# Kernel tuning notes

Measured on AMD Instinct MI355X. Metric: run time of the kernel, lower is better.

The kernel has to match this reference:

```python
import jax, jax.numpy as jnp
import numpy as np

B, S, D, F, E, K = 4, 2048, 512, 2048, 8, 2


def setup_inputs() -> dict:
    key = jax.random.key(0)
    kx, kg, kw, kv, k2 = jax.random.split(key, 5)
    scale = 0.02
    return {
        "x": jax.random.normal(kx, (B, S, D), dtype=jnp.float32),
        "Wg": jax.random.normal(kg, (D, E), dtype=jnp.float32) * scale,
        "W": jax.random.normal(kw, (E, D, F), dtype=jnp.float32) * scale,
        "V": jax.random.normal(kv, (E, D, F), dtype=jnp.float32) * scale,
        "W2": jax.random.normal(k2, (E, F, D), dtype=jnp.float32) * scale,
    }


def reference(x, Wg, W, V, W2):
    # Gating: top-k over expert logits, softmax over the selected k logits.
    gate_logits = jnp.einsum("bsd,de->bse", x, Wg)                 # [B,S,E]
    topv, topi = jax.lax.top_k(gate_logits, K)                      # [B,S,K]
    w = jax.nn.softmax(topv, axis=-1)                               # [B,S,K]
    # Dense per-token combine weights: gw[b,s,e] = sum_k w[b,s,k]*[topi[b,s,k]==e]
    gw = jnp.sum(w[..., None] * jax.nn.one_hot(topi, E, dtype=x.dtype), axis=-2)  # [B,S,E]

    y = jnp.zeros_like(x)
    n_experts = W.shape[0]
    for e in range(n_experts):  # fixed small loop over experts
        h = jax.nn.silu(jnp.einsum("bsd,df->bsf", x, W[e])) * jnp.einsum("bsd,df->bsf", x, V[e])
        y = y + gw[..., e:e + 1] * jnp.einsum("bsf,fd->bsd", h, W2[e])
    return y
```

## Files before the change

kernel.cpp:

```cpp
#include <hip/hip_runtime.h>
#include <hip/hip_bf16.h>
#include <stdint.h>

#define TT 8192
#define DD 512
#define FF 2048
#define EE 8
#define MAXT 136

typedef __attribute__((ext_vector_type(8))) short bf16x8;
typedef __attribute__((ext_vector_type(4))) float f32x4;

static __device__ __forceinline__ unsigned short f2b(float f) {
  union { __hip_bfloat16 b; unsigned short u; } cv;
  cv.b = __float2bfloat16(f);
  return cv.u;
}
static __device__ __forceinline__ float b2f(unsigned short u) {
  union { unsigned int i; float f; } cv;
  cv.i = ((unsigned int)u) << 16;
  return cv.f;
}

static __device__ __forceinline__ void gload16(const void* g, void* l) {
  __builtin_amdgcn_global_load_lds(
      (const __attribute__((address_space(1))) unsigned int*)g,
      (__attribute__((address_space(3))) unsigned int*)l, 16, 0, 0);
}

#define VMCNT12 asm volatile("s_waitcnt vmcnt(12)" ::: "memory")
#define VMCNT6  asm volatile("s_waitcnt vmcnt(6)" ::: "memory")
#define VMCNT0  asm volatile("s_waitcnt vmcnt(0)" ::: "memory")
#define BARX    asm volatile("s_barrier" ::: "memory")

__launch_bounds__(256)
__global__ void k_prep(const float* __restrict__ x, const float* __restrict__ Wg,
                       unsigned short* __restrict__ xb,
                       int* __restrict__ te, float* __restrict__ tw) {
  int wid = threadIdx.x >> 6, lane = threadIdx.x & 63;
  int t = blockIdx.x * 4 + wid;
  const float* xr = x + (size_t)t * DD;
  unsigned short* xbr = xb + (size_t)t * DD;
  int d0 = lane * 8;

  float4 v0 = *(const float4*)(xr + d0);
  float4 v1 = *(const float4*)(xr + d0 + 4);
  ushort4 o0, o1;
  o0.x = f2b(v0.x); o0.y = f2b(v0.y); o0.z = f2b(v0.z); o0.w = f2b(v0.w);
  o1.x = f2b(v1.x); o1.y = f2b(v1.y); o1.z = f2b(v1.z); o1.w = f2b(v1.w);
  *(ushort4*)(xbr + d0) = o0;
  *(ushort4*)(xbr + d0 + 4) = o1;

  float xv[8] = {v0.x, v0.y, v0.z, v0.w, v1.x, v1.y, v1.z, v1.w};
  float acc[EE];
#pragma unroll
  for (int e = 0; e < EE; e++) acc[e] = 0.f;
#pragma unroll
  for (int j = 0; j < 8; j++) {
    const float* wg = Wg + (size_t)(d0 + j) * EE;
    float4 a = *(const float4*)wg;
    float4 b = *(const float4*)(wg + 4);
    acc[0] += xv[j] * a.x; acc[1] += xv[j] * a.y; acc[2] += xv[j] * a.z; acc[3] += xv[j] * a.w;
    acc[4] += xv[j] * b.x; acc[5] += xv[j] * b.y; acc[6] += xv[j] * b.z; acc[7] += xv[j] * b.w;
  }
#pragma unroll
  for (int e = 0; e < EE; e++)
    for (int o = 32; o; o >>= 1) acc[e] += __shfl_xor(acc[e], o);
  if (lane == 0) {
    int e1 = 0; float v1m = acc[0];
#pragma unroll
    for (int e = 1; e < EE; e++) if (acc[e] > v1m) { v1m = acc[e]; e1 = e; }
    int e2 = -1; float v2m = -INFINITY;
#pragma unroll
    for (int e = 0; e < EE; e++) if (e != e1 && acc[e] > v2m) { v2m = acc[e]; e2 = e; }
    float ex = __expf(v2m - v1m);
    float w1 = 1.f / (1.f + ex);
    float w2 = ex / (1.f + ex);
    te[t * 2] = e1; te[t * 2 + 1] = e2;
    tw[t * 2] = w1; tw[t * 2 + 1] = w2;
  }
}

__global__ void k_tcvt_all(const float* __restrict__ W, const float* __restrict__ V,
                           const float* __restrict__ W2, unsigned short* __restrict__ Wt,
                           unsigned short* __restrict__ Vt, unsigned short* __restrict__ W2t) {
  __shared__ float tile[32][33];
  int z = blockIdx.y;
  const float* src; unsigned short* dst; int N, nbx;
  if (z < 16) {
    int e = z & 7;
    size_t base = (size_t)e * DD * FF;
    src = (z < 8 ? W : V) + base;
    dst = (z < 8 ? Wt : Vt) + base;
    N = FF; nbx = FF / 32;
  } else {
    int e = z - 16;
    size_t base = (size_t)e * DD * FF;
    src = W2 + base; dst = W2t + base;
    N = DD; nbx = DD / 32;
  }
  int M = (z < 16) ? DD : FF;
  int bx = blockIdx.x;
  int cb = (bx % nbx) * 32, rb = (bx / nbx) * 32;
  int tx = threadIdx.x, ty = threadIdx.y;
#pragma unroll
  for (int i = 0; i < 4; i++)
    tile[ty + i * 8][tx] = src[(size_t)(rb + ty + i * 8) * N + cb + tx];
  __syncthreads();
#pragma unroll
  for (int i = 0; i < 4; i++)
    dst[(size_t)(cb + ty + i * 8) * M + rb + tx] = f2b(tile[tx][ty + i * 8]);
}

__launch_bounds__(1024)
__global__ void k_route(const int* __restrict__ te, const float* __restrict__ tw,
                        int* __restrict__ ctrl, int* __restrict__ perm,
                        float* __restrict__ pw, int* __restrict__ tileE,
                        int* __restrict__ tileRow, int* __restrict__ inv) {
  __shared__ int wsum[17][EE];
  __shared__ int ebase[EE];
  int tid = threadIdx.x;
  int lane = tid & 63, wid = tid >> 6;
  int myte[16]; float mytw[16];
  int c[EE];
#pragma unroll
  for (int e = 0; e < EE; e++) c[e] = 0;
  int s0 = tid * 16;
#pragma unroll
  for (int j = 0; j < 16; j++) {
    myte[j] = te[s0 + j];
    mytw[j] = tw[s0 + j];
#pragma unroll
    for (int e = 0; e < EE; e++) if (myte[j] == e) c[e]++;
  }
  int incl[EE];
#pragma unroll
  for (int e = 0; e < EE; e++) incl[e] = c[e];
  for (int off = 1; off < 64; off <<= 1) {
#pragma unroll
    for (int e = 0; e < EE; e++) {
      int v = __shfl_up(incl[e], off);
      if (lane >= off) incl[e] += v;
    }
  }
  if (lane == 63)
#pragma unroll
    for (int e = 0; e < EE; e++) wsum[wid][e] = incl[e];
  __syncthreads();
  if (tid < EE) {
    int s = 0;
    for (int w = 0; w < 16; w++) { int v = wsum[w][tid]; wsum[w][tid] = s; s += v; }
    wsum[16][tid] = s;
  }
  __syncthreads();
  if (tid == 0) {
    int s = 0, nt = 0;
    for (int e = 0; e < EE; e++) {
      int cnt = wsum[16][e];
      ebase[e] = s; ctrl[8 + e] = s; ctrl[e] = cnt;
      for (int i = 0; i < cnt; i += 128) { tileE[nt] = e; tileRow[nt] = s + i; nt++; }
      s += cnt;
    }
    ctrl[16] = s; ctrl[17] = nt;
  }
  __syncthreads();
#pragma unroll
  for (int e = 0; e < EE; e++) {
    int p = ebase[e] + wsum[wid][e] + incl[e] - c[e];
#pragma unroll
    for (int j = 0; j < 16; j++) {
      if (myte[j] == e) {
        perm[p] = (s0 + j) >> 1;
        pw[p] = mytw[j];
        inv[s0 + j] = p;
        p++;
      }
    }
  }
}

__launch_bounds__(256, 2)
__global__ void k_ffn1(const unsigned short* __restrict__ xb,
                       const unsigned short* __restrict__ Wt,
                       const unsigned short* __restrict__ Vt,
                       const int* __restrict__ perm, const float* __restrict__ pw,
                       const int* __restrict__ ctrl, const int* __restrict__ tileE,
                       const int* __restrict__ tileRow,
                       unsigned short* __restrict__ h) {
  int ti = blockIdx.y;
  if (ti >= ctrl[17]) return;
  int e = tileE[ti];
  int row0 = tileRow[ti];
  int last = ctrl[8 + e] + ctrl[e] - 1;
  int f0 = blockIdx.x * 128;

  __shared__ __align__(16) short As[3][128 * 32];
  __shared__ __align__(16) short Bs[3][256 * 32];

  int tid = threadIdx.x;
  int lane = tid & 63, wid = tid >> 6;
  int wr = wid >> 1, wc = wid & 1;

  int sl = (((tid & 3) ^ ((tid >> 3) & 3))) * 8;

  int ar1 = row0 + (tid >> 2); if (ar1 > last) ar1 = last;
  int ar2 = row0 + (tid >> 2) + 64; if (ar2 > last) ar2 = last;
  const unsigned short* agp1 = xb + (size_t)perm[ar1] * DD + sl;
  const unsigned short* agp2 = xb + (size_t)perm[ar2] * DD + sl;
  const unsigned short* wgp1 = Wt + ((size_t)e * FF + f0 + (tid >> 2)) * DD + sl;
  const unsigned short* wgp2 = wgp1 + (size_t)64 * DD;
  const unsigned short* vgp1 = Vt + ((size_t)e * FF + f0 + (tid >> 2)) * DD + sl;
  const unsigned short* vgp2 = vgp1 + (size_t)64 * DD;

#define STAGE1(buf, k0) do { \
    gload16(agp1 + (k0), &As[buf][tid * 8]); \
    gload16(agp2 + (k0), &As[buf][(tid + 256) * 8]); \
    gload16(wgp1 + (k0), &Bs[buf][tid * 8]); \
    gload16(wgp2 + (k0), &Bs[buf][(tid + 256) * 8]); \
    gload16(vgp1 + (k0), &Bs[buf][(tid + 512) * 8]); \
    gload16(vgp2 + (k0), &Bs[buf][(tid + 768) * 8]); \
  } while (0)

  f32x4 zz = {0.f, 0.f, 0.f, 0.f};
  f32x4 accw[4][4], accv[4][4];
#pragma unroll
  for (int m = 0; m < 4; m++)
#pragma unroll
    for (int n = 0; n < 4; n++) { accw[m][n] = zz; accv[m][n] = zz; }

  int lrow = lane & 15;
  int jx = (((lane >> 4) ^ ((lane >> 1) & 3))) * 8;

#define COMP1(buf) do { \
    bf16x8 a[4], bw[4], bv[4]; \
    _Pragma("unroll") \
    for (int m = 0; m < 4; m++) a[m] = *(bf16x8*)&As[buf][(wr * 64 + m * 16 + lrow) * 32 + jx]; \
    _Pragma("unroll") \
    for (int n = 0; n < 4; n++) { \
      bw[n] = *(bf16x8*)&Bs[buf][(wc * 64 + n * 16 + lrow) * 32 + jx]; \
      bv[n] = *(bf16x8*)&Bs[buf][(128 + wc * 64 + n * 16 + lrow) * 32 + jx]; \
    } \
    _Pragma("unroll") \
    for (int m = 0; m < 4; m++) \
      _Pragma("unroll") \
      for (int n = 0; n < 4; n++) { \
        accw[m][n] = __builtin_amdgcn_mfma_f32_16x16x32_bf16(a[m], bw[n], accw[m][n], 0, 0, 0); \
        accv[m][n] = __builtin_amdgcn_mfma_f32_16x16x32_bf16(a[m], bv[n], accv[m][n], 0, 0, 0); \
      } \
  } while (0)

  STAGE1(0, 0); STAGE1(1, 32); STAGE1(2, 64);
#pragma unroll 1
  for (int kt = 0; kt < 4; kt++) {
    VMCNT12; BARX; COMP1(0); BARX; STAGE1(0, (kt * 3 + 3) * 32);
    VMCNT12; BARX; COMP1(1); BARX; STAGE1(1, (kt * 3 + 4) * 32);
    VMCNT12; BARX; COMP1(2); BARX; STAGE1(2, (kt * 3 + 5) * 32);
  }
  VMCNT12; BARX; COMP1(0); BARX; STAGE1(0, 15 * 32);
  VMCNT12; BARX; COMP1(1);
  VMCNT6;  BARX; COMP1(2);
  VMCNT0;  BARX; COMP1(0);
#undef STAGE1
#undef COMP1

#pragma unroll
  for (int m = 0; m < 4; m++) {
    int rbase = row0 + wr * 64 + m * 16 + (lane >> 4) * 4;
#pragma unroll
    for (int reg = 0; reg < 4; reg++) {
      int r = rbase + reg;
      if (r > last) continue;
      float pwv = pw[r];
      size_t hrow = (size_t)r * FF;
#pragma unroll
      for (int n = 0; n < 4; n++) {
        float a = accw[m][n][reg];
        float b = accv[m][n][reg];
        float hv = a / (1.f + __expf(-a)) * b * pwv;
        h[hrow + f0 + wc * 64 + n * 16 + lrow] = f2b(hv);
      }
    }
  }
}

__launch_bounds__(256)
__global__ void k_ffn2(const unsigned short* __restrict__ h,
                       const unsigned short* __restrict__ W2t,
                       const int* __restrict__ ctrl,
                       const int* __restrict__ tileE, const int* __restrict__ tileRow,
                       unsigned short* __restrict__ yp) {
  int ti = blockIdx.y;
  if (ti >= ctrl[17]) return;
  int e = tileE[ti];
  int row0 = tileRow[ti];
  int last = ctrl[8 + e] + ctrl[e] - 1;
  int d0 = blockIdx.x * 128;

  __shared__ __align__(16) short As[2][128 * 32];
  __shared__ __align__(16) short Bs[2][128 * 32];

  int tid = threadIdx.x;
  int lane = tid & 63, wid = tid >> 6;
  int wm = (wid >> 1) * 64, wn = (wid & 1) * 64;

  int sl = (((tid & 3) ^ ((tid >> 3) & 3))) * 8;

  int ar1 = row0 + (tid >> 2); if (ar1 > last) ar1 = last;
  int ar2 = row0 + (tid >> 2) + 64; if (ar2 > last) ar2 = last;
  const unsigned short* agp1 = h + (size_t)ar1 * FF + sl;
  const unsigned short* agp2 = h + (size_t)ar2 * FF + sl;
  const unsigned short* bgp1 = W2t + ((size_t)e * DD + d0 + (tid >> 2)) * FF + sl;
  const unsigned short* bgp2 = bgp1 + (size_t)64 * FF;

#define STAGE2(buf, k0) do { \
    gload16(agp1 + (k0), &As[buf][tid * 8]); \
    gload16(agp2 + (k0), &As[buf][(tid + 256) * 8]); \
    gload16(bgp1 + (k0), &Bs[buf][tid * 8]); \
    gload16(bgp2 + (k0), &Bs[buf][(tid + 256) * 8]); \
  } while (0)

  f32x4 zz = {0.f, 0.f, 0.f, 0.f};
  f32x4 acc[4][4];
#pragma unroll
  for (int m = 0; m < 4; m++)
#pragma unroll
    for (int n = 0; n < 4; n++) acc[m][n] = zz;

  int lrow = lane & 15;
  int jx = (((lane >> 4) ^ ((lane >> 1) & 3))) * 8;

#define COMP2(buf) do { \
    bf16x8 a[4], b[4]; \
    _Pragma("unroll") \
    for (int m = 0; m < 4; m++) a[m] = *(bf16x8*)&As[buf][(wm + m * 16 + lrow) * 32 + jx]; \
    _Pragma("unroll") \
    for (int n = 0; n < 4; n++) b[n] = *(bf16x8*)&Bs[buf][(wn + n * 16 + lrow) * 32 + jx]; \
    _Pragma("unroll") \
    for (int m = 0; m < 4; m++) \
      _Pragma("unroll") \
      for (int n = 0; n < 4; n++) \
        acc[m][n] = __builtin_amdgcn_mfma_f32_16x16x32_bf16(a[m], b[n], acc[m][n], 0, 0, 0); \
  } while (0)

  STAGE2(0, 0);
  __syncthreads();
#pragma unroll 1
  for (int ks = 0; ks < 64; ks += 2) {
    if (ks + 1 < 64) STAGE2(1, (ks + 1) * 32);
    COMP2(0);
    __syncthreads();
    if (ks + 2 < 64) STAGE2(0, (ks + 2) * 32);
    COMP2(1);
    __syncthreads();
  }
#undef STAGE2
#undef COMP2

#pragma unroll
  for (int m = 0; m < 4; m++) {
    int rbase = row0 + wm + m * 16 + (lane >> 4) * 4;
#pragma unroll
    for (int reg = 0; reg < 4; reg++) {
      int r = rbase + reg;
      if (r > last) continue;
      unsigned short* ypr = yp + (size_t)r * DD + d0;
#pragma unroll
      for (int n = 0; n < 4; n++)
        ypr[wn + n * 16 + lrow] = f2b(acc[m][n][reg]);
    }
  }
}

__launch_bounds__(256)
__global__ void k_gather(const unsigned short* __restrict__ yp,
                         const int* __restrict__ inv, float* __restrict__ y) {
  int i = blockIdx.x * 256 + threadIdx.x;
  int t = i >> 6, seg = (i & 63) * 8;
  int pa = inv[2 * t], pb = inv[2 * t + 1];
  bf16x8 a = *(const bf16x8*)(yp + (size_t)pa * DD + seg);
  bf16x8 b = *(const bf16x8*)(yp + (size_t)pb * DD + seg);
  float* yr = y + (size_t)t * DD + seg;
  float4 o0, o1;
  o0.x = b2f((unsigned short)a[0]) + b2f((unsigned short)b[0]);
  o0.y = b2f((unsigned short)a[1]) + b2f((unsigned short)b[1]);
  o0.z = b2f((unsigned short)a[2]) + b2f((unsigned short)b[2]);
  o0.w = b2f((unsigned short)a[3]) + b2f((unsigned short)b[3]);
  o1.x = b2f((unsigned short)a[4]) + b2f((unsigned short)b[4]);
  o1.y = b2f((unsigned short)a[5]) + b2f((unsigned short)b[5]);
  o1.z = b2f((unsigned short)a[6]) + b2f((unsigned short)b[6]);
  o1.w = b2f((unsigned short)a[7]) + b2f((unsigned short)b[7]);
  *(float4*)yr = o0;
  *(float4*)(yr + 4) = o1;
}

extern "C" void kernel_launch(void* const* d_in, const int* in_sizes, int n_in,
                              void* d_out, int out_size, void* d_ws, size_t ws_size,
                              hipStream_t stream) {
  const float* x  = (const float*)d_in[0];
  const float* Wg = (const float*)d_in[1];
  const float* W  = (const float*)d_in[2];
  const float* V  = (const float*)d_in[3];
  const float* W2 = (const float*)d_in[4];
  float* y = (float*)d_out;

  char* ws = (char*)d_ws;
  size_t off = 0;
  auto alloc = [&](size_t n) -> char* {
    char* p = ws + off;
    off += (n + 255) & ~(size_t)255;
    return p;
  };
  unsigned short* xb  = (unsigned short*)alloc((size_t)TT * DD * 2);
  unsigned short* Wt  = (unsigned short*)alloc((size_t)EE * DD * FF * 2);
  unsigned short* Vt  = (unsigned short*)alloc((size_t)EE * DD * FF * 2);
  unsigned short* W2t = (unsigned short*)alloc((size_t)EE * DD * FF * 2);
  unsigned short* h   = (unsigned short*)alloc((size_t)TT * 2 * FF * 2);
  int*   perm = (int*)alloc(TT * 2 * 4);
  float* pw   = (float*)alloc(TT * 2 * 4);
  int*   te   = (int*)alloc(TT * 2 * 4);
  float* tw   = (float*)alloc(TT * 2 * 4);
  int*   inv  = (int*)alloc(TT * 2 * 4);
  int*   ctrl = (int*)alloc(256);
  int*   tileE   = (int*)alloc(MAXT * 4);
  int*   tileRow = (int*)alloc(MAXT * 4);
  if (off > ws_size) return;

  unsigned short* yp = (unsigned short*)Wt;

  k_prep<<<TT / 4, 256, 0, stream>>>(x, Wg, xb, te, tw);
  k_tcvt_all<<<dim3(1024, 24), dim3(32, 8), 0, stream>>>(W, V, W2, Wt, Vt, W2t);
  k_route<<<1, 1024, 0, stream>>>(te, tw, ctrl, perm, pw, tileE, tileRow, inv);
  k_ffn1<<<dim3(FF / 128, MAXT), 256, 0, stream>>>(xb, Wt, Vt, perm, pw, ctrl, tileE, tileRow, h);
  k_ffn2<<<dim3(DD / 128, MAXT), 256, 0, stream>>>(h, W2t, ctrl, tileE, tileRow, yp);
  k_gather<<<TT * 64 / 256, 256, 0, stream>>>(yp, inv, y);
}
```

Measured before the change: 238.7 us.

## Enlarge FFN1 tiles to 256 rows with 8-wave ping-pong pipelined GEMM

Rewrites the first expert GEMM kernel to use 256-row token tiles, 512 threads, BK=64 and double-buffered 128 KB dynamic LDS. Loads are interleaved with MFMA phases, and s_setprio raises priority around the MFMA bursts. Routing now emits a second tile list sized for 256-row tiles. The aim is better operand reuse and more overlap of memory traffic with compute. In exchange, padding waste on partial expert tiles grows and occupancy drops because of the large LDS footprint and extra barriers.

```diff
diff --git a/kernel.cpp b/kernel.cpp
--- a/kernel.cpp
+++ b/kernel.cpp
@@ -7,6 +7,7 @@
 #define FF 2048
 #define EE 8
 #define MAXT 136
+#define MAXT2 72
 
 typedef __attribute__((ext_vector_type(8))) short bf16x8;
 typedef __attribute__((ext_vector_type(4))) float f32x4;
@@ -28,10 +29,11 @@
       (__attribute__((address_space(3))) unsigned int*)l, 16, 0, 0);
 }
 
-#define VMCNT12 asm volatile("s_waitcnt vmcnt(12)" ::: "memory")
-#define VMCNT6  asm volatile("s_waitcnt vmcnt(6)" ::: "memory")
+#define VMCNT4  asm volatile("s_waitcnt vmcnt(4)" ::: "memory")
 #define VMCNT0  asm volatile("s_waitcnt vmcnt(0)" ::: "memory")
 #define BARX    asm volatile("s_barrier" ::: "memory")
+#define PRIO1   __builtin_amdgcn_s_setprio(1)
+#define PRIO0   __builtin_amdgcn_s_setprio(0)
 
 __launch_bounds__(256)
 __global__ void k_prep(const float* __restrict__ x, const float* __restrict__ Wg,
@@ -116,7 +118,8 @@
 __global__ void k_route(const int* __restrict__ te, const float* __restrict__ tw,
                         int* __restrict__ ctrl, int* __restrict__ perm,
                         float* __restrict__ pw, int* __restrict__ tileE,
-                        int* __restrict__ tileRow, int* __restrict__ inv) {
+                        int* __restrict__ tileRow, int* __restrict__ inv,
+                        int* __restrict__ tileE2, int* __restrict__ tileRow2) {
   __shared__ int wsum[17][EE];
   __shared__ int ebase[EE];
   int tid = threadIdx.x;
@@ -154,14 +157,15 @@
   }
   __syncthreads();
   if (tid == 0) {
-    int s = 0, nt = 0;
+    int s = 0, nt = 0, nt2 = 0;
     for (int e = 0; e < EE; e++) {
       int cnt = wsum[16][e];
       ebase[e] = s; ctrl[8 + e] = s; ctrl[e] = cnt;
       for (int i = 0; i < cnt; i += 128) { tileE[nt] = e; tileRow[nt] = s + i; nt++; }
+      for (int i = 0; i < cnt; i += 256) { tileE2[nt2] = e; tileRow2[nt2] = s + i; nt2++; }
       s += cnt;
     }
-    ctrl[16] = s; ctrl[17] = nt;
+    ctrl[16] = s; ctrl[17] = nt; ctrl[18] = nt2;
   }
   __syncthreads();
 #pragma unroll
@@ -179,93 +183,150 @@
   }
 }
 
-__launch_bounds__(256, 2)
+__launch_bounds__(512, 2)
 __global__ void k_ffn1(const unsigned short* __restrict__ xb,
                        const unsigned short* __restrict__ Wt,
                        const unsigned short* __restrict__ Vt,
                        const int* __restrict__ perm, const float* __restrict__ pw,
-                       const int* __restrict__ ctrl, const int* __restrict__ tileE,
-                       const int* __restrict__ tileRow,
+                       const int* __restrict__ ctrl, const int* __restrict__ tileE2,
+                       const int* __restrict__ tileRow2,
                        unsigned short* __restrict__ h) {
   int ti = blockIdx.y;
-  if (ti >= ctrl[17]) return;
-  int e = tileE[ti];
-  int row0 = tileRow[ti];
+  if (ti >= ctrl[18]) return;
+  int e = tileE2[ti];
+  int row0 = tileRow2[ti];
   int last = ctrl[8 + e] + ctrl[e] - 1;
   int f0 = blockIdx.x * 128;
 
-  __shared__ __align__(16) short As[3][128 * 32];
-  __shared__ __align__(16) short Bs[3][256 * 32];
-
-  int tid = threadIdx.x;
-  int lane = tid & 63, wid = tid >> 6;
-  int wr = wid >> 1, wc = wid & 1;
-
-  int sl = (((tid & 3) ^ ((tid >> 3) & 3))) * 8;
-
-  int ar1 = row0 + (tid >> 2); if (ar1 > last) ar1 = last;
-  int ar2 = row0 + (tid >> 2) + 64; if (ar2 > last) ar2 = last;
-  const unsigned short* agp1 = xb + (size_t)perm[ar1] * DD + sl;
-  const unsigned short* agp2 = xb + (size_t)perm[ar2] * DD + sl;
-  const unsigned short* wgp1 = Wt + ((size_t)e * FF + f0 + (tid >> 2)) * DD + sl;
-  const unsigned short* wgp2 = wgp1 + (size_t)64 * DD;
-  const unsigned short* vgp1 = Vt + ((size_t)e * FF + f0 + (tid >> 2)) * DD + sl;
-  const unsigned short* vgp2 = vgp1 + (size_t)64 * DD;
-
-#define STAGE1(buf, k0) do { \
-    gload16(agp1 + (k0), &As[buf][tid * 8]); \
-    gload16(agp2 + (k0), &As[buf][(tid + 256) * 8]); \
-    gload16(wgp1 + (k0), &Bs[buf][tid * 8]); \
-    gload16(wgp2 + (k0), &Bs[buf][(tid + 256) * 8]); \
-    gload16(vgp1 + (k0), &Bs[buf][(tid + 512) * 8]); \
-    gload16(vgp2 + (k0), &Bs[buf][(tid + 768) * 8]); \
+  extern __shared__ short lds[];
+  short* As0 = lds;
+  short* As1 = lds + 16384;
+  short* Bs0 = lds + 32768;
+  short* Bs1 = lds + 49152;
+
+  int t = threadIdx.x;
+  int lane = t & 63, wid = t >> 6;
+  int wr = wid >> 2, wc = wid & 3;
+  int lrow = lane & 15, lk = lane >> 4, l7 = lane & 7;
+
+  int w64 = t >> 3;
+  int lsl = ((t & 7) ^ (w64 & 7)) * 8;
+  int dof0 = (w64 + 0) * 64 + (t & 7) * 8;
+  int dof1 = (w64 + 64) * 64 + (t & 7) * 8;
+  int dof2 = (w64 + 128) * 64 + (t & 7) * 8;
+  int dof3 = (w64 + 192) * 64 + (t & 7) * 8;
+  int ar0 = row0 + w64;        if (ar0 > last) ar0 = last;
+  int ar1 = row0 + w64 + 64;   if (ar1 > last) ar1 = last;
+  int ar2 = row0 + w64 + 128;  if (ar2 > last) ar2 = last;
+  int ar3 = row0 + w64 + 192;  if (ar3 > last) ar3 = last;
+  const unsigned short* ap0 = xb + (size_t)perm[ar0] * DD + lsl;
+  const unsigned short* ap1 = xb + (size_t)perm[ar1] * DD + lsl;
+  const unsigned short* ap2 = xb + (size_t)perm[ar2] * DD + lsl;
+  const unsigned short* ap3 = xb + (size_t)perm[ar3] * DD + lsl;
+  const unsigned short* bbase = ((w64 < 32) ? Wt : Vt)
+      + ((size_t)e * FF + f0 + (w64 & 31)) * DD + lsl;
+
+#define SA0(Ad, kt) do { gload16(ap0 + (kt) * 64, &Ad[dof0]); \
+                         gload16(ap1 + (kt) * 64, &Ad[dof1]); } while (0)
+#define SA1(Ad, kt) do { gload16(ap2 + (kt) * 64, &Ad[dof2]); \
+                         gload16(ap3 + (kt) * 64, &Ad[dof3]); } while (0)
+#define SB0(Bd, kt) do { gload16(bbase + (kt) * 64,            &Bd[dof0]); \
+                         gload16(bbase + 32 * DD + (kt) * 64,  &Bd[dof1]); } while (0)
+#define SB1(Bd, kt) do { gload16(bbase + 64 * DD + (kt) * 64,  &Bd[dof2]); \
+                         gload16(bbase + 96 * DD + (kt) * 64,  &Bd[dof3]); } while (0)
+
+  bf16x8 af[4][2], bfw[2][2], bfv[2][2];
+  f32x4 zz = {0.f, 0.f, 0.f, 0.f};
+  f32x4 accw[8][2], accv[8][2];
+#pragma unroll
+  for (int m = 0; m < 8; m++)
+#pragma unroll
+    for (int n = 0; n < 2; n++) { accw[m][n] = zz; accv[m][n] = zz; }
+
+#define AREAD(Ad, mh) do { \
+    _Pragma("unroll") \
+    for (int m_ = 0; m_ < 4; m_++) \
+      _Pragma("unroll") \
+      for (int ks_ = 0; ks_ < 2; ks_++) \
+        af[m_][ks_] = *(bf16x8*)&Ad[(wr * 128 + ((mh) * 4 + m_) * 16 + lrow) * 64 + ((ks_ * 4 + lk) ^ l7) * 8]; \
   } while (0)
-
-  f32x4 zz = {0.f, 0.f, 0.f, 0.f};
-  f32x4 accw[4][4], accv[4][4];
-#pragma unroll
-  for (int m = 0; m < 4; m++)
-#pragma unroll
-    for (int n = 0; n < 4; n++) { accw[m][n] = zz; accv[m][n] = zz; }
-
-  int lrow = lane & 15;
-  int jx = (((lane >> 4) ^ ((lane >> 1) & 3))) * 8;
-
-#define COMP1(buf) do { \
-    bf16x8 a[4], bw[4], bv[4]; \
-    _Pragma("unroll") \
-    for (int m = 0; m < 4; m++) a[m] = *(bf16x8*)&As[buf][(wr * 64 + m * 16 + lrow) * 32 + jx]; \
-    _Pragma("unroll") \
-    for (int n = 0; n < 4; n++) { \
-      bw[n] = *(bf16x8*)&Bs[buf][(wc * 64 + n * 16 + lrow) * 32 + jx]; \
-      bv[n] = *(bf16x8*)&Bs[buf][(128 + wc * 64 + n * 16 + lrow) * 32 + jx]; \
-    } \
-    _Pragma("unroll") \
-    for (int m = 0; m < 4; m++) \
+#define BWREAD(Bd) do { \
+    _Pragma("unroll") \
+    for (int n_ = 0; n_ < 2; n_++) \
       _Pragma("unroll") \
-      for (int n = 0; n < 4; n++) { \
-        accw[m][n] = __builtin_amdgcn_mfma_f32_16x16x32_bf16(a[m], bw[n], accw[m][n], 0, 0, 0); \
-        accv[m][n] = __builtin_amdgcn_mfma_f32_16x16x32_bf16(a[m], bv[n], accv[m][n], 0, 0, 0); \
-      } \
+      for (int ks_ = 0; ks_ < 2; ks_++) \
+        bfw[n_][ks_] = *(bf16x8*)&Bd[(wc * 64 + n_ * 16 + lrow) * 64 + ((ks_ * 4 + lk) ^ l7) * 8]; \
   } while (0)
-
-  STAGE1(0, 0); STAGE1(1, 32); STAGE1(2, 64);
+#define BVREAD(Bd) do { \
+    _Pragma("unroll") \
+    for (int n_ = 0; n_ < 2; n_++) \
+      _Pragma("unroll") \
+      for (int ks_ = 0; ks_ < 2; ks_++) \
+        bfv[n_][ks_] = *(bf16x8*)&Bd[(wc * 64 + 32 + n_ * 16 + lrow) * 64 + ((ks_ * 4 + lk) ^ l7) * 8]; \
+  } while (0)
+#define MFW(mh) do { PRIO1; \
+    _Pragma("unroll") \
+    for (int m_ = 0; m_ < 4; m_++) \
+      _Pragma("unroll") \
+      for (int n_ = 0; n_ < 2; n_++) \
+        _Pragma("unroll") \
+        for (int ks_ = 0; ks_ < 2; ks_++) \
+          accw[(mh) * 4 + m_][n_] = __builtin_amdgcn_mfma_f32_16x16x32_bf16(af[m_][ks_], bfw[n_][ks_], accw[(mh) * 4 + m_][n_], 0, 0, 0); \
+    PRIO0; } while (0)
+#define MFV(mh) do { PRIO1; \
+    _Pragma("unroll") \
+    for (int m_ = 0; m_ < 4; m_++) \
+      _Pragma("unroll") \
+      for (int n_ = 0; n_ < 2; n_++) \
+        _Pragma("unroll") \
+        for (int ks_ = 0; ks_ < 2; ks_++) \
+          accv[(mh) * 4 + m_][n_] = __builtin_amdgcn_mfma_f32_16x16x32_bf16(af[m_][ks_], bfv[n_][ks_], accv[(mh) * 4 + m_][n_], 0, 0, 0); \
+    PRIO0; } while (0)
+
+  SB0(Bs0, 0); SB1(Bs0, 0); SA0(As0, 0); SA1(As0, 0);
+  SB0(Bs1, 1); SB1(Bs1, 1);
+  VMCNT4; BARX;
+
 #pragma unroll 1
-  for (int kt = 0; kt < 4; kt++) {
-    VMCNT12; BARX; COMP1(0); BARX; STAGE1(0, (kt * 3 + 3) * 32);
-    VMCNT12; BARX; COMP1(1); BARX; STAGE1(1, (kt * 3 + 4) * 32);
-    VMCNT12; BARX; COMP1(2); BARX; STAGE1(2, (kt * 3 + 5) * 32);
-  }
-  VMCNT12; BARX; COMP1(0); BARX; STAGE1(0, 15 * 32);
-  VMCNT12; BARX; COMP1(1);
-  VMCNT6;  BARX; COMP1(2);
-  VMCNT0;  BARX; COMP1(0);
-#undef STAGE1
-#undef COMP1
-
-#pragma unroll
-  for (int m = 0; m < 4; m++) {
-    int rbase = row0 + wr * 64 + m * 16 + (lane >> 4) * 4;
+  for (int i = 0; i < 4; i++) {
+    int kt1 = 2 * i + 1, kt2 = 2 * i + 2, kt3 = 2 * i + 3;
+    bool nl = (i < 3);
+    AREAD(As0, 0); BWREAD(Bs0);
+    SA0(As1, kt1);
+    BARX; MFW(0); BARX;
+    BVREAD(Bs0);
+    SA1(As1, kt1);
+    BARX; MFV(0); BARX;
+    AREAD(As0, 1);
+    if (nl) SB0(Bs0, kt2);
+    BARX; MFV(1); BARX;
+    if (nl) { SB1(Bs0, kt2); VMCNT4; } else { VMCNT0; }
+    BARX; MFW(1); BARX;
+    AREAD(As1, 0); BWREAD(Bs1);
+    if (nl) SA0(As0, kt2);
+    BARX; MFW(0); BARX;
+    BVREAD(Bs1);
+    if (nl) SA1(As0, kt2);
+    BARX; MFV(0); BARX;
+    AREAD(As1, 1);
+    if (nl) SB0(Bs1, kt3);
+    BARX; MFV(1); BARX;
+    if (nl) { SB1(Bs1, kt3); VMCNT4; } else { VMCNT0; }
+    BARX; MFW(1); BARX;
+  }
+#undef SA0
+#undef SA1
+#undef SB0
+#undef SB1
+#undef AREAD
+#undef BWREAD
+#undef BVREAD
+#undef MFW
+#undef MFV
+
+#pragma unroll
+  for (int mf = 0; mf < 8; mf++) {
+    int rbase = row0 + wr * 128 + mf * 16 + lk * 4;
 #pragma unroll
     for (int reg = 0; reg < 4; reg++) {
       int r = rbase + reg;
@@ -273,11 +334,11 @@
       float pwv = pw[r];
       size_t hrow = (size_t)r * FF;
 #pragma unroll
-      for (int n = 0; n < 4; n++) {
-        float a = accw[m][n][reg];
-        float b = accv[m][n][reg];
+      for (int nf = 0; nf < 2; nf++) {
+        float a = accw[mf][nf][reg];
+        float b = accv[mf][nf][reg];
         float hv = a / (1.f + __expf(-a)) * b * pwv;
-        h[hrow + f0 + wc * 64 + n * 16 + lrow] = f2b(hv);
+        h[hrow + f0 + wc * 32 + nf * 16 + lrow] = f2b(hv);
       }
     }
   }
@@ -421,16 +482,21 @@
   float* tw   = (float*)alloc(TT * 2 * 4);
   int*   inv  = (int*)alloc(TT * 2 * 4);
   int*   ctrl = (int*)alloc(256);
-  int*   tileE   = (int*)alloc(MAXT * 4);
-  int*   tileRow = (int*)alloc(MAXT * 4);
+  int*   tileE    = (int*)alloc(MAXT * 4);
+  int*   tileRow  = (int*)alloc(MAXT * 4);
+  int*   tileE2   = (int*)alloc(MAXT2 * 4);
+  int*   tileRow2 = (int*)alloc(MAXT2 * 4);
   if (off > ws_size) return;
 
   unsigned short* yp = (unsigned short*)Wt;
+
+  hipFuncSetAttribute((const void*)k_ffn1,
+                      hipFuncAttributeMaxDynamicSharedMemorySize, 131072);
 
   k_prep<<<TT / 4, 256, 0, stream>>>(x, Wg, xb, te, tw);
   k_tcvt_all<<<dim3(1024, 24), dim3(32, 8), 0, stream>>>(W, V, W2, Wt, Vt, W2t);
-  k_route<<<1, 1024, 0, stream>>>(te, tw, ctrl, perm, pw, tileE, tileRow, inv);
-  k_ffn1<<<dim3(FF / 128, MAXT), 256, 0, stream>>>(xb, Wt, Vt, perm, pw, ctrl, tileE, tileRow, h);
+  k_route<<<1, 1024, 0, stream>>>(te, tw, ctrl, perm, pw, tileE, tileRow, inv, tileE2, tileRow2);
+  k_ffn1<<<dim3(FF / 128, MAXT2), 512, 131072, stream>>>(xb, Wt, Vt, perm, pw, ctrl, tileE2, tileRow2, h);
   k_ffn2<<<dim3(DD / 128, MAXT), 256, 0, stream>>>(h, W2t, ctrl, tileE, tileRow, yp);
   k_gather<<<TT * 64 / 256, 256, 0, stream>>>(yp, inv, y);
 }
```

Result: slower. 251.0 us (+5.1%).

## Split FFN2 reduction dimension across two blocks and sum partials in gather

Applied to the files above, without the earlier changes.

The second expert GEMM now splits its 2048-long reduction into two halves along a new grid z dimension, doubling the number of blocks. Each half writes its own bf16 partial output into a separate region of the scratch buffer. The gather kernel reads both partials for each routed pair and adds them. This raises occupancy for the small-N GEMM (only 4 column tiles), at the cost of twice the partial-output traffic, a second rounding to bf16, and scratch space aliased onto the Wt buffer.

```diff
diff --git a/kernel.cpp b/kernel.cpp
--- a/kernel.cpp
+++ b/kernel.cpp
@@ -295,6 +295,8 @@
   int row0 = tileRow[ti];
   int last = ctrl[8 + e] + ctrl[e] - 1;
   int d0 = blockIdx.x * 128;
+  int kh = blockIdx.z;
+  int kb = kh * 1024;
 
   __shared__ __align__(16) short As[2][128 * 32];
   __shared__ __align__(16) short Bs[2][128 * 32];
@@ -307,9 +309,9 @@
 
   int ar1 = row0 + (tid >> 2); if (ar1 > last) ar1 = last;
   int ar2 = row0 + (tid >> 2) + 64; if (ar2 > last) ar2 = last;
-  const unsigned short* agp1 = h + (size_t)ar1 * FF + sl;
-  const unsigned short* agp2 = h + (size_t)ar2 * FF + sl;
-  const unsigned short* bgp1 = W2t + ((size_t)e * DD + d0 + (tid >> 2)) * FF + sl;
+  const unsigned short* agp1 = h + (size_t)ar1 * FF + kb + sl;
+  const unsigned short* agp2 = h + (size_t)ar2 * FF + kb + sl;
+  const unsigned short* bgp1 = W2t + ((size_t)e * DD + d0 + (tid >> 2)) * FF + kb + sl;
   const unsigned short* bgp2 = bgp1 + (size_t)64 * FF;
 
 #define STAGE2(buf, k0) do { \
@@ -345,11 +347,11 @@
   STAGE2(0, 0);
   __syncthreads();
 #pragma unroll 1
-  for (int ks = 0; ks < 64; ks += 2) {
-    if (ks + 1 < 64) STAGE2(1, (ks + 1) * 32);
+  for (int ks = 0; ks < 32; ks += 2) {
+    STAGE2(1, (ks + 1) * 32);
     COMP2(0);
     __syncthreads();
-    if (ks + 2 < 64) STAGE2(0, (ks + 2) * 32);
+    if (ks + 2 < 32) STAGE2(0, (ks + 2) * 32);
     COMP2(1);
     __syncthreads();
   }
@@ -363,7 +365,7 @@
     for (int reg = 0; reg < 4; reg++) {
       int r = rbase + reg;
       if (r > last) continue;
-      unsigned short* ypr = yp + (size_t)r * DD + d0;
+      unsigned short* ypr = yp + ((size_t)kh * (TT * 2) + r) * DD + d0;
 #pragma unroll
       for (int n = 0; n < 4; n++)
         ypr[wn + n * 16 + lrow] = f2b(acc[m][n][reg]);
@@ -377,18 +379,21 @@
   int i = blockIdx.x * 256 + threadIdx.x;
   int t = i >> 6, seg = (i & 63) * 8;
   int pa = inv[2 * t], pb = inv[2 * t + 1];
-  bf16x8 a = *(const bf16x8*)(yp + (size_t)pa * DD + seg);
-  bf16x8 b = *(const bf16x8*)(yp + (size_t)pb * DD + seg);
+  const unsigned short* y1 = yp + (size_t)(TT * 2) * DD;
+  bf16x8 a0 = *(const bf16x8*)(yp + (size_t)pa * DD + seg);
+  bf16x8 b0 = *(const bf16x8*)(yp + (size_t)pb * DD + seg);
+  bf16x8 a1 = *(const bf16x8*)(y1 + (size_t)pa * DD + seg);
+  bf16x8 b1 = *(const bf16x8*)(y1 + (size_t)pb * DD + seg);
   float* yr = y + (size_t)t * DD + seg;
   float4 o0, o1;
-  o0.x = b2f((unsigned short)a[0]) + b2f((unsigned short)b[0]);
-  o0.y = b2f((unsigned short)a[1]) + b2f((unsigned short)b[1]);
-  o0.z = b2f((unsigned short)a[2]) + b2f((unsigned short)b[2]);
-  o0.w = b2f((unsigned short)a[3]) + b2f((unsigned short)b[3]);
-  o1.x = b2f((unsigned short)a[4]) + b2f((unsigned short)b[4]);
-  o1.y = b2f((unsigned short)a[5]) + b2f((unsigned short)b[5]);
-  o1.z = b2f((unsigned short)a[6]) + b2f((unsigned short)b[6]);
-  o1.w = b2f((unsigned short)a[7]) + b2f((unsigned short)b[7]);
+  o0.x = (b2f((unsigned short)a0[0]) + b2f((unsigned short)a1[0])) + (b2f((unsigned short)b0[0]) + b2f((unsigned short)b1[0]));
+  o0.y = (b2f((unsigned short)a0[1]) + b2f((unsigned short)a1[1])) + (b2f((unsigned short)b0[1]) + b2f((unsigned short)b1[1]));
+  o0.z = (b2f((unsigned short)a0[2]) + b2f((unsigned short)a1[2])) + (b2f((unsigned short)b0[2]) + b2f((unsigned short)b1[2]));
+  o0.w = (b2f((unsigned short)a0[3]) + b2f((unsigned short)a1[3])) + (b2f((unsigned short)b0[3]) + b2f((unsigned short)b1[3]));
+  o1.x = (b2f((unsigned short)a0[4]) + b2f((unsigned short)a1[4])) + (b2f((unsigned short)b0[4]) + b2f((unsigned short)b1[4]));
+  o1.y = (b2f((unsigned short)a0[5]) + b2f((unsigned short)a1[5])) + (b2f((unsigned short)b0[5]) + b2f((unsigned short)b1[5]));
+  o1.z = (b2f((unsigned short)a0[6]) + b2f((unsigned short)a1[6])) + (b2f((unsigned short)b0[6]) + b2f((unsigned short)b1[6]));
+  o1.w = (b2f((unsigned short)a0[7]) + b2f((unsigned short)a1[7])) + (b2f((unsigned short)b0[7]) + b2f((unsigned short)b1[7]));
   *(float4*)yr = o0;
   *(float4*)(yr + 4) = o1;
 }
@@ -431,6 +436,6 @@
   k_tcvt_all<<<dim3(1024, 24), dim3(32, 8), 0, stream>>>(W, V, W2, Wt, Vt, W2t);
   k_route<<<1, 1024, 0, stream>>>(te, tw, ctrl, perm, pw, tileE, tileRow, inv);
   k_ffn1<<<dim3(FF / 128, MAXT), 256, 0, stream>>>(xb, Wt, Vt, perm, pw, ctrl, tileE, tileRow, h);
-  k_ffn2<<<dim3(DD / 128, MAXT), 256, 0, stream>>>(h, W2t, ctrl, tileE, tileRow, yp);
+  k_ffn2<<<dim3(DD / 128, MAXT, 2), 256, 0, stream>>>(h, W2t, ctrl, tileE, tileRow, yp);
   k_gather<<<TT * 64 / 256, 256, 0, stream>>>(yp, inv, y);
 }
```

Result: no change. 240.4 us (+0.7%).
